# Performance work log

Measured on AMD Instinct MI355X. Metric: run time of the kernel, lower is better.

The kernel has to match this reference:

```python
import jax, jax.numpy as jnp
from jax import lax
import numpy as np


def _relu(x):
    return jnp.maximum(x, 0)


def setup_inputs() -> dict:
    key = jax.random.key(0)
    ks = jax.random.split(key, 20)
    B = 1024
    s = 0.05  # small init scale
    d = {
        "raw_input": jax.random.normal(ks[0], (B, 1, 28, 28), jnp.float32),
        "output_embed": jax.random.normal(ks[1], (B, 512), jnp.float32),
        "latent_embed": jax.random.normal(ks[2], (B, 512), jnp.float32),
        "conv1_w": jax.random.normal(ks[3], (16, 1, 3, 3), jnp.float32) * s,
        "conv1_b": jax.random.normal(ks[4], (16,), jnp.float32) * s,
        "conv2_w": jax.random.normal(ks[5], (32, 16, 3, 3), jnp.float32) * s,
        "conv2_b": jax.random.normal(ks[6], (32,), jnp.float32) * s,
        "proj_w1": jax.random.normal(ks[7], (1568, 1024), jnp.float32) * s,
        "proj_b1": jax.random.normal(ks[8], (1024,), jnp.float32) * s,
        "proj_w2": jax.random.normal(ks[9], (1024, 512), jnp.float32) * s,
        "proj_b2": jax.random.normal(ks[10], (512,), jnp.float32) * s,
        "bb_w1": jax.random.normal(ks[11], (512, 1024), jnp.float32) * s,
        "bb_b1": jax.random.normal(ks[12], (1024,), jnp.float32) * s,
        "bb_w2": jax.random.normal(ks[13], (1024, 512), jnp.float32) * s,
        "bb_b2": jax.random.normal(ks[14], (512,), jnp.float32) * s,
        "head_w": jax.random.normal(ks[15], (512, 10), jnp.float32) * s,
        "head_b": jax.random.normal(ks[16], (10,), jnp.float32) * s,
        "Nsup": 16,
        "n_latent": 6,
    }
    return d


def _maxpool2(x):
    # 2x2 max pool, stride 2, NCHW
    return lax.reduce_window(x, -jnp.inf, lax.max, (1, 1, 2, 2), (1, 1, 2, 2), "VALID")


def reference(raw_input, output_embed, latent_embed,
              conv1_w, conv1_b, conv2_w, conv2_b,
              proj_w1, proj_b1, proj_w2, proj_b2,
              bb_w1, bb_b1, bb_w2, bb_b2,
              head_w, head_b, Nsup, n_latent):
    dn = ("NCHW", "OIHW", "NCHW")
    B = raw_input.shape[0]

    def backbone(x):
        return _relu(_relu(x @ bb_w1 + bb_b1) @ bb_w2 + bb_b2)

    def latent_recursion(inp, out, lat, n):
        if n > 0:
            for _ in range(n):
                lat = backbone(inp + out + lat)
            out = backbone(lat + inp)
        else:
            out = backbone(inp + out + lat)
        return out, lat

    # CNN extractor + input embedding projection (B, 512)
    x = _relu(lax.conv_general_dilated(raw_input, conv1_w, (1, 1), "SAME",
                                       dimension_numbers=dn) + conv1_b[None, :, None, None])
    x = _maxpool2(x)  # (B,16,14,14)
    x = _relu(lax.conv_general_dilated(x, conv2_w, (1, 1), "SAME",
                                       dimension_numbers=dn) + conv2_b[None, :, None, None])
    x = _maxpool2(x)  # (B,32,7,7)
    h = x.reshape(B, -1)  # (B, 1568)
    inp = _relu(_relu(h @ proj_w1 + proj_b1) @ proj_w2 + proj_b2)  # (B,512)

    sg = lax.stop_gradient
    out, lat = output_embed, latent_embed
    T = 3
    logits = None
    for _ in range(Nsup):
        # deep_recursion: T-1 no-grad latent recursions, then one tracked
        for _ in range(T - 1):
            out, lat = latent_recursion(inp, out, lat, n_latent)
            out, lat = sg(out), sg(lat)
        out, lat = latent_recursion(inp, out, lat, n_latent)
        logits = out @ head_w + head_b
        out, lat = sg(out), sg(lat)
    return logits
```

## Files before the change

### kernel.cpp

```cpp
#include <hip/hip_runtime.h>
#include <hip/hip_bf16.h>


typedef unsigned short ushort_t;
typedef __attribute__((ext_vector_type(8))) short short8;
typedef __attribute__((ext_vector_type(4))) float f32x4;

__device__ inline unsigned f2bf_rne(float v) {
    unsigned u = __float_as_uint(v);
    return (u + 0x7fffu + ((u >> 16) & 1u)) >> 16;
}
__device__ inline void split2(float v, ushort_t& h, ushort_t& l) {
    unsigned uh = f2bf_rne(v);
    h = (ushort_t)uh;
    float fh = __uint_as_float(uh << 16);
    l = (ushort_t)f2bf_rne(v - fh);
}

__global__ __launch_bounds__(256) void conv1_pool(
    const float* __restrict__ in, const float* __restrict__ w,
    const float* __restrict__ bias, float* __restrict__ out)
{
    int idx = blockIdx.x * 256 + threadIdx.x;
    int xo = idx % 14; int t = idx / 14;
    int yo = t % 14;  t /= 14;
    int oc = t % 16;  int b = t / 16;
    const float* ip = in + (size_t)b * 784;
    const float* wp = w + oc * 9;
    float win[4][4];
#pragma unroll
    for (int yy = 0; yy < 4; ++yy)
#pragma unroll
        for (int xx = 0; xx < 4; ++xx) {
            int y = 2 * yo + yy - 1, x = 2 * xo + xx - 1;
            win[yy][xx] = (y >= 0 && y < 28 && x >= 0 && x < 28) ? ip[y * 28 + x] : 0.f;
        }
    float bs = bias[oc];
    float m = -1e30f;
#pragma unroll
    for (int py = 0; py < 2; ++py)
#pragma unroll
        for (int px = 0; px < 2; ++px) {
            float s = bs;
#pragma unroll
            for (int dy = 0; dy < 3; ++dy)
#pragma unroll
                for (int dx = 0; dx < 3; ++dx)
                    s = fmaf(win[py + dy][px + dx], wp[dy * 3 + dx], s);
            m = fmaxf(m, s);
        }
    out[idx] = fmaxf(m, 0.f);
}

__global__ __launch_bounds__(256) void conv2_pool(
    const float* __restrict__ in, const float* __restrict__ w,
    const float* __restrict__ bias, float* __restrict__ out)
{
    __shared__ float ws_[32 * 16 * 9];
    for (int i = threadIdx.x; i < 4608; i += 256) ws_[i] = w[i];
    __syncthreads();
    int idx = blockIdx.x * 256 + threadIdx.x;
    int xo = idx % 7; int t = idx / 7;
    int yo = t % 7;  t /= 7;
    int oc = t % 32; int b = t / 32;
    const float* ip = in + (size_t)b * 16 * 196;
    float bs = bias[oc];
    float s00 = bs, s01 = bs, s10 = bs, s11 = bs;
    for (int ic = 0; ic < 16; ++ic) {
        const float* ipp = ip + ic * 196;
        float win[4][4];
#pragma unroll
        for (int yy = 0; yy < 4; ++yy)
#pragma unroll
            for (int xx = 0; xx < 4; ++xx) {
                int y = 2 * yo + yy - 1, x = 2 * xo + xx - 1;
                win[yy][xx] = (y >= 0 && y < 14 && x >= 0 && x < 14) ? ipp[y * 14 + x] : 0.f;
            }
        const float* wp = ws_ + (oc * 16 + ic) * 9;
#pragma unroll
        for (int dy = 0; dy < 3; ++dy)
#pragma unroll
            for (int dx = 0; dx < 3; ++dx) {
                float wv = wp[dy * 3 + dx];
                s00 = fmaf(win[0 + dy][0 + dx], wv, s00);
                s01 = fmaf(win[0 + dy][1 + dx], wv, s01);
                s10 = fmaf(win[1 + dy][0 + dx], wv, s10);
                s11 = fmaf(win[1 + dy][1 + dx], wv, s11);
            }
    }
    float m = fmaxf(fmaxf(s00, s01), fmaxf(s10, s11));
    out[idx] = fmaxf(m, 0.f);
}

#define BMF 64
#define BNF 64
#define BKF 16

__global__ __launch_bounds__(256) void gemm_f32(
    const float* __restrict__ A0, const float* __restrict__ W,
    const float* __restrict__ bias, float* __restrict__ C,
    int M, int N, int K)
{
    __shared__ float As[BKF][BMF];
    __shared__ float Bs[BKF][BNF];
    const int tid = threadIdx.x;
    const int tx = tid % 16;
    const int ty = tid / 16;
    const int row0 = blockIdx.y * BMF;
    const int col0 = blockIdx.x * BNF;
    float acc[4][4] = {};
    const int ra = tid / 4;
    const int ca = 4 * (tid % 4);
    const int rb = tid / 16;
    const int cb = 4 * (tid % 16);
    for (int k0 = 0; k0 < K; k0 += BKF) {
        float4 v = *(const float4*)(A0 + (size_t)(row0 + ra) * K + k0 + ca);
        float4 bvec = *(const float4*)(W + (size_t)(k0 + rb) * N + col0 + cb);
        As[ca + 0][ra] = v.x;
        As[ca + 1][ra] = v.y;
        As[ca + 2][ra] = v.z;
        As[ca + 3][ra] = v.w;
        *(float4*)&Bs[rb][cb] = bvec;
        __syncthreads();
#pragma unroll
        for (int kk = 0; kk < BKF; ++kk) {
            float4 av = *(const float4*)&As[kk][ty * 4];
            float4 bv = *(const float4*)&Bs[kk][tx * 4];
            float a_[4] = {av.x, av.y, av.z, av.w};
            float b_[4] = {bv.x, bv.y, bv.z, bv.w};
#pragma unroll
            for (int i = 0; i < 4; ++i)
#pragma unroll
                for (int j = 0; j < 4; ++j)
                    acc[i][j] = fmaf(a_[i], b_[j], acc[i][j]);
        }
        __syncthreads();
    }
    float4 bv = *(const float4*)(bias + col0 + tx * 4);
    float bb[4] = {bv.x, bv.y, bv.z, bv.w};
#pragma unroll
    for (int i = 0; i < 4; ++i) {
        float4 o;
        o.x = fmaxf(acc[i][0] + bb[0], 0.f);
        o.y = fmaxf(acc[i][1] + bb[1], 0.f);
        o.z = fmaxf(acc[i][2] + bb[2], 0.f);
        o.w = fmaxf(acc[i][3] + bb[3], 0.f);
        *(float4*)(C + (size_t)(row0 + ty * 4 + i) * N + col0 + tx * 4) = o;
    }
}

__global__ __launch_bounds__(256) void prep_wt(
    const float* __restrict__ w, ushort_t* __restrict__ th,
    ushort_t* __restrict__ tl, int K, int N)
{
    int idx = blockIdx.x * 256 + threadIdx.x;
    int n = idx / K, k = idx % K;
    float v = w[(size_t)k * N + n];
    split2(v, th[idx], tl[idx]);
}

__global__ __launch_bounds__(256) void init_xs(
    const float* __restrict__ inpf, const float* __restrict__ oute,
    const float* __restrict__ late, float* __restrict__ io,
    ushort_t* __restrict__ xh, ushort_t* __restrict__ xl)
{
    int i = blockIdx.x * 256 + threadIdx.x;
    float t = inpf[i] + oute[i];
    io[i] = t;
    split2(t + late[i], xh[i], xl[i]);
}

__global__ void init_bar(unsigned* bar) {
    bar[threadIdx.x] = 0;
    bar[threadIdx.x + 256] = 0;
}

__device__ __forceinline__ void group_barrier(unsigned* bar, int g,
                                              unsigned& tgt)
{
    __syncthreads();
    if (threadIdx.x == 0) {
        __builtin_amdgcn_fence(__ATOMIC_RELEASE, "workgroup");
        __hip_atomic_fetch_add(bar + g * 32, 1u, __ATOMIC_RELAXED,
                               __HIP_MEMORY_SCOPE_AGENT);
        while (__hip_atomic_load(bar + g * 32, __ATOMIC_RELAXED,
                                 __HIP_MEMORY_SCOPE_AGENT) < tgt)
            __builtin_amdgcn_s_sleep(1);
        __builtin_amdgcn_fence(__ATOMIC_ACQUIRE, "workgroup");
        asm volatile("buffer_inv sc0" ::: "memory");
    }
    tgt += 32;
    __syncthreads();
}

__device__ __forceinline__ short8 afrag(const ushort_t* __restrict__ p,
                                        int row, int K, int kpos)
{
    return *(const short8*)(p + (size_t)row * K + kpos);
}

__global__ __launch_bounds__(512, 2) void trm_persist(
    ushort_t* __restrict__ xs_hi, ushort_t* __restrict__ xs_lo,
    ushort_t* __restrict__ h1_hi, ushort_t* __restrict__ h1_lo,
    const ushort_t* __restrict__ W1h, const ushort_t* __restrict__ W1l,
    const ushort_t* __restrict__ W2h, const ushort_t* __restrict__ W2l,
    const float* __restrict__ bb1, const float* __restrict__ bb2,
    float* __restrict__ io, const float* __restrict__ inpf,
    float* __restrict__ latf, float* __restrict__ outf,
    const float* __restrict__ hw, const float* __restrict__ hb,
    float* __restrict__ logits, unsigned* bar)
{
    __shared__ __align__(16) unsigned char w1lds[65536];
    __shared__ __align__(16) unsigned char w2lds[65536];
    __shared__ int sh_gs;

    const int tid = threadIdx.x;
    const int w = tid >> 6, lane = tid & 63;
    const int q = lane >> 4, li = lane & 15;

    if (tid == 0) {
        unsigned xcc;
        asm volatile("s_getreg_b32 %0, hwreg(HW_REG_XCC_ID)" : "=s"(xcc));
        xcc &= 7u;
        unsigned s = __hip_atomic_fetch_add(bar + 384 + xcc * 8, 1u,
                                            __ATOMIC_RELAXED,
                                            __HIP_MEMORY_SCOPE_AGENT);
        sh_gs = (int)((xcc << 8) | (s & 31u));
    }
    __syncthreads();
    const int g = sh_gs >> 8;
    const int slot = sh_gs & 255;
    const int c1 = slot * 32;
    const int c2 = slot * 16;
    const int rowA = g * 128 + w * 16;

    for (int i = tid; i < 4096; i += 512) {
        int comp = i >> 11;
        int rem = i & 2047;
        int n = rem >> 6, c = rem & 63;
        const ushort_t* src = (comp ? W1l : W1h) + (size_t)(c1 + n) * 512 + c * 8;
        int dst = ((((comp << 4) + (c >> 2)) * 2 + (n >> 4)) * 64 +
                   ((c & 3) * 16 + (n & 15))) * 16;
        *(uint4*)(w1lds + dst) = *(const uint4*)src;
    }
    for (int i = tid; i < 4096; i += 512) {
        int comp = i >> 11;
        int rem = i & 2047;
        int n = rem >> 7, c = rem & 127;
        const ushort_t* src = (comp ? W2l : W2h) + (size_t)(c2 + n) * 1024 + c * 8;
        int dst = (((comp << 5) + (c >> 2)) * 64 + ((c & 3) * 16 + n)) * 16;
        *(uint4*)(w2lds + dst) = *(const uint4*)src;
    }
    __syncthreads();

    float bias1[2];
    bias1[0] = bb1[c1 + li];
    bias1[1] = bb1[c1 + 16 + li];
    float bias2 = bb2[c2 + li];
    unsigned tgt = 32;

    for (int step = 0; step < 336; ++step) {
        {
            f32x4 acc0 = {}, acc1 = {};
            short8 aF[4][2];
#pragma unroll
            for (int p = 0; p < 4; ++p) {
                int kp = p * 32 + q * 8;
                aF[p][0] = afrag(xs_hi, rowA + li, 512, kp);
                aF[p][1] = afrag(xs_lo, rowA + li, 512, kp);
            }
#pragma unroll
            for (int s = 0; s < 16; ++s) {
                short8 ah = aF[s & 3][0], al = aF[s & 3][1];
                if (s + 4 < 16) {
                    int kp = (s + 4) * 32 + q * 8;
                    aF[(s + 4) & 3][0] = afrag(xs_hi, rowA + li, 512, kp);
                    aF[(s + 4) & 3][1] = afrag(xs_lo, rowA + li, 512, kp);
                }
                const int base = (s * 2 * 64 + lane) * 16;
                short8 bh0 = *(const short8*)(w1lds + base);
                short8 bh1 = *(const short8*)(w1lds + base + 1024);
                short8 bl0 = *(const short8*)(w1lds + 32768 + base);
                short8 bl1 = *(const short8*)(w1lds + 32768 + base + 1024);
                acc0 = __builtin_amdgcn_mfma_f32_16x16x32_bf16(ah, bh0, acc0, 0, 0, 0);
                acc0 = __builtin_amdgcn_mfma_f32_16x16x32_bf16(ah, bl0, acc0, 0, 0, 0);
                acc0 = __builtin_amdgcn_mfma_f32_16x16x32_bf16(al, bh0, acc0, 0, 0, 0);
                acc0 = __builtin_amdgcn_mfma_f32_16x16x32_bf16(al, bl0, acc0, 0, 0, 0);
                acc1 = __builtin_amdgcn_mfma_f32_16x16x32_bf16(ah, bh1, acc1, 0, 0, 0);
                acc1 = __builtin_amdgcn_mfma_f32_16x16x32_bf16(ah, bl1, acc1, 0, 0, 0);
                acc1 = __builtin_amdgcn_mfma_f32_16x16x32_bf16(al, bh1, acc1, 0, 0, 0);
                acc1 = __builtin_amdgcn_mfma_f32_16x16x32_bf16(al, bl1, acc1, 0, 0, 0);
            }
#pragma unroll
            for (int tj = 0; tj < 2; ++tj) {
                int colg = c1 + tj * 16 + li;
                float bv = bias1[tj];
#pragma unroll
                for (int rr = 0; rr < 4; ++rr) {
                    int rowg = rowA + q * 4 + rr;
                    size_t idx = (size_t)rowg * 1024 + colg;
                    float v = fmaxf((tj ? acc1[rr] : acc0[rr]) + bv, 0.f);
                    split2(v, h1_hi[idx], h1_lo[idx]);
                }
            }
        }
        group_barrier(bar, g, tgt);

        {
            int im = step % 7;
            int mode = (im < 5) ? 1 : ((im == 5) ? 2 : 3);
            f32x4 acc = {};
            short8 aF[4][2];
#pragma unroll
            for (int p = 0; p < 4; ++p) {
                int kp = p * 32 + q * 8;
                aF[p][0] = afrag(h1_hi, rowA + li, 1024, kp);
                aF[p][1] = afrag(h1_lo, rowA + li, 1024, kp);
            }
#pragma unroll
            for (int s = 0; s < 32; ++s) {
                short8 ah = aF[s & 3][0], al = aF[s & 3][1];
                if (s + 4 < 32) {
                    int kp = (s + 4) * 32 + q * 8;
                    aF[(s + 4) & 3][0] = afrag(h1_hi, rowA + li, 1024, kp);
                    aF[(s + 4) & 3][1] = afrag(h1_lo, rowA + li, 1024, kp);
                }
                const int base = (s * 64 + lane) * 16;
                short8 bh = *(const short8*)(w2lds + base);
                short8 bl = *(const short8*)(w2lds + 32768 + base);
                acc = __builtin_amdgcn_mfma_f32_16x16x32_bf16(ah, bh, acc, 0, 0, 0);
                acc = __builtin_amdgcn_mfma_f32_16x16x32_bf16(ah, bl, acc, 0, 0, 0);
                acc = __builtin_amdgcn_mfma_f32_16x16x32_bf16(al, bh, acc, 0, 0, 0);
                acc = __builtin_amdgcn_mfma_f32_16x16x32_bf16(al, bl, acc, 0, 0, 0);
            }
            int colg = c2 + li;
#pragma unroll
            for (int rr = 0; rr < 4; ++rr) {
                int rowg = rowA + q * 4 + rr;
                size_t idx = (size_t)rowg * 512 + colg;
                float v = fmaxf(acc[rr] + bias2, 0.f);
                if (mode == 1) {
                    split2(io[idx] + v, xs_hi[idx], xs_lo[idx]);
                } else if (mode == 2) {
                    split2(inpf[idx] + v, xs_hi[idx], xs_lo[idx]);
                    latf[idx] = v;
                } else {
                    outf[idx] = v;
                    float t2 = inpf[idx] + v;
                    io[idx] = t2;
                    split2(t2 + latf[idx], xs_hi[idx], xs_lo[idx]);
                }
            }
        }
        group_barrier(bar, g, tgt);
    }

    {
        int idx = slot * 512 + tid;
        if (idx < 1280) {
            int rloc = idx / 10, j = idx % 10;
            int row = g * 128 + rloc;
            const float* r = outf + (size_t)row * 512;
            float s = hb[j];
            for (int k = 0; k < 512; ++k) s = fmaf(r[k], hw[k * 10 + j], s);
            logits[row * 10 + j] = s;
        }
    }
}

extern "C" void kernel_launch(void* const* d_in, const int* in_sizes, int n_in,
                              void* d_out, int out_size, void* d_ws, size_t ws_size,
                              hipStream_t stream)
{
    const float* raw   = (const float*)d_in[0];
    const float* out_e = (const float*)d_in[1];
    const float* lat_e = (const float*)d_in[2];
    const float* c1w = (const float*)d_in[3];
    const float* c1b = (const float*)d_in[4];
    const float* c2w = (const float*)d_in[5];
    const float* c2b = (const float*)d_in[6];
    const float* pw1 = (const float*)d_in[7];
    const float* pb1 = (const float*)d_in[8];
    const float* pw2 = (const float*)d_in[9];
    const float* pb2 = (const float*)d_in[10];
    const float* bw1 = (const float*)d_in[11];
    const float* bb1 = (const float*)d_in[12];
    const float* bw2 = (const float*)d_in[13];
    const float* bb2 = (const float*)d_in[14];
    const float* hw  = (const float*)d_in[15];
    const float* hb  = (const float*)d_in[16];

    char* base = (char*)d_ws;
    float*    pool1  = (float*)   (base + 0);
    ushort_t* h1_hi  = (ushort_t*)(base + 0);
    ushort_t* h1_lo  = (ushort_t*)(base + 2097152);
    ushort_t* xs_hi  = (ushort_t*)(base + 4194304);
    ushort_t* xs_lo  = (ushort_t*)(base + 5242880);
    float*    io     = (float*)   (base + 6291456);
    float*    latf   = (float*)   (base + 8388608);
    float*    h1f    = (float*)   (base + 0);
    float*    h      = (float*)   (base + 12845056);
    float*    inpf   = (float*)   (base + 19267584);
    float*    outf   = (float*)   (base + 21364736);
    ushort_t* bW1t_h = (ushort_t*)(base + 23461888);
    ushort_t* bW1t_l = (ushort_t*)(base + 24510464);
    ushort_t* bW2t_h = (ushort_t*)(base + 25559040);
    ushort_t* bW2t_l = (ushort_t*)(base + 26607616);
    unsigned* bar    = (unsigned*)(base + 27656192);

    prep_wt<<<2048, 256, 0, stream>>>(bw1, bW1t_h, bW1t_l, 512, 1024);
    prep_wt<<<2048, 256, 0, stream>>>(bw2, bW2t_h, bW2t_l, 1024, 512);
    init_bar<<<1, 256, 0, stream>>>(bar);

    conv1_pool<<<3211264 / 256, 256, 0, stream>>>(raw, c1w, c1b, pool1);
    conv2_pool<<<1605632 / 256, 256, 0, stream>>>(pool1, c2w, c2b, h);
    gemm_f32<<<dim3(16, 16), 256, 0, stream>>>(h, pw1, pb1, h1f, 1024, 1024, 1568);
    gemm_f32<<<dim3(8, 16), 256, 0, stream>>>(h1f, pw2, pb2, inpf, 1024, 512, 1024);
    init_xs<<<2048, 256, 0, stream>>>(inpf, out_e, lat_e, io, xs_hi, xs_lo);

    trm_persist<<<256, 512, 0, stream>>>(
        xs_hi, xs_lo, h1_hi, h1_lo, bW1t_h, bW1t_l, bW2t_h, bW2t_l,
        bb1, bb2, io, inpf, latf, outf, hw, hb, (float*)d_out, bar);
}
```

Before: 8.440 ms.

## Pack hi/lo bf16 activations interleaved and drop lo*lo MFMA term

Activation hi/lo bf16 splits are now stored interleaved in one 32-bit word per element, so each fragment comes from a single contiguous global load and is unpacked with byte permutes. The lo*lo product term, which contributes negligibly to the result, is also dropped from both backbone GEMMs, cutting MFMA count per k-step from 4 to 3. Each unpack adds some VALU work, and accuracy drops slightly.

```diff
diff --git a/kernel.cpp b/kernel.cpp
--- a/kernel.cpp
+++ b/kernel.cpp
@@ -15,6 +15,31 @@
     h = (ushort_t)uh;
     float fh = __uint_as_float(uh << 16);
     l = (ushort_t)f2bf_rne(v - fh);
+}
+__device__ inline unsigned split2pk(float v) {
+    unsigned uh = f2bf_rne(v);
+    float fh = __uint_as_float(uh << 16);
+    unsigned ul = f2bf_rne(v - fh);
+    return (ul << 16) | uh;
+}
+
+union S8U { short8 s; unsigned u[4]; };
+__device__ __forceinline__ void unpk(uint4 u0, uint4 u1, short8& h, short8& l) {
+    S8U a, b;
+    a.u[0] = __builtin_amdgcn_perm(u0.y, u0.x, 0x05040100u);
+    b.u[0] = __builtin_amdgcn_perm(u0.y, u0.x, 0x07060302u);
+    a.u[1] = __builtin_amdgcn_perm(u0.w, u0.z, 0x05040100u);
+    b.u[1] = __builtin_amdgcn_perm(u0.w, u0.z, 0x07060302u);
+    a.u[2] = __builtin_amdgcn_perm(u1.y, u1.x, 0x05040100u);
+    b.u[2] = __builtin_amdgcn_perm(u1.y, u1.x, 0x07060302u);
+    a.u[3] = __builtin_amdgcn_perm(u1.w, u1.z, 0x05040100u);
+    b.u[3] = __builtin_amdgcn_perm(u1.w, u1.z, 0x07060302u);
+    h = a.s; l = b.s;
+}
+__device__ __forceinline__ void ldpk(const unsigned* __restrict__ p, int row,
+                                     int K, int kpos, uint4& u0, uint4& u1) {
+    const uint4* q = (const uint4*)(p + (size_t)row * K + kpos);
+    u0 = q[0]; u1 = q[1];
 }
 
 __global__ __launch_bounds__(256) void conv1_pool(
@@ -162,12 +187,12 @@
 __global__ __launch_bounds__(256) void init_xs(
     const float* __restrict__ inpf, const float* __restrict__ oute,
     const float* __restrict__ late, float* __restrict__ io,
-    ushort_t* __restrict__ xh, ushort_t* __restrict__ xl)
+    unsigned* __restrict__ xs_pk)
 {
     int i = blockIdx.x * 256 + threadIdx.x;
     float t = inpf[i] + oute[i];
     io[i] = t;
-    split2(t + late[i], xh[i], xl[i]);
+    xs_pk[i] = split2pk(t + late[i]);
 }
 
 __global__ void init_bar(unsigned* bar) {
@@ -193,15 +218,8 @@
     __syncthreads();
 }
 
-__device__ __forceinline__ short8 afrag(const ushort_t* __restrict__ p,
-                                        int row, int K, int kpos)
-{
-    return *(const short8*)(p + (size_t)row * K + kpos);
-}
-
 __global__ __launch_bounds__(512, 2) void trm_persist(
-    ushort_t* __restrict__ xs_hi, ushort_t* __restrict__ xs_lo,
-    ushort_t* __restrict__ h1_hi, ushort_t* __restrict__ h1_lo,
+    unsigned* __restrict__ xs_pk, unsigned* __restrict__ h1_pk,
     const ushort_t* __restrict__ W1h, const ushort_t* __restrict__ W1l,
     const ushort_t* __restrict__ W2h, const ushort_t* __restrict__ W2l,
     const float* __restrict__ bb1, const float* __restrict__ bb2,
@@ -262,21 +280,17 @@
     for (int step = 0; step < 336; ++step) {
         {
             f32x4 acc0 = {}, acc1 = {};
-            short8 aF[4][2];
-#pragma unroll
-            for (int p = 0; p < 4; ++p) {
-                int kp = p * 32 + q * 8;
-                aF[p][0] = afrag(xs_hi, rowA + li, 512, kp);
-                aF[p][1] = afrag(xs_lo, rowA + li, 512, kp);
-            }
+            uint4 aR[4][2];
+#pragma unroll
+            for (int p = 0; p < 4; ++p)
+                ldpk(xs_pk, rowA + li, 512, p * 32 + q * 8, aR[p][0], aR[p][1]);
 #pragma unroll
             for (int s = 0; s < 16; ++s) {
-                short8 ah = aF[s & 3][0], al = aF[s & 3][1];
-                if (s + 4 < 16) {
-                    int kp = (s + 4) * 32 + q * 8;
-                    aF[(s + 4) & 3][0] = afrag(xs_hi, rowA + li, 512, kp);
-                    aF[(s + 4) & 3][1] = afrag(xs_lo, rowA + li, 512, kp);
-                }
+                short8 ah, al;
+                unpk(aR[s & 3][0], aR[s & 3][1], ah, al);
+                if (s + 4 < 16)
+                    ldpk(xs_pk, rowA + li, 512, (s + 4) * 32 + q * 8,
+                         aR[(s + 4) & 3][0], aR[(s + 4) & 3][1]);
                 const int base = (s * 2 * 64 + lane) * 16;
                 short8 bh0 = *(const short8*)(w1lds + base);
                 short8 bh1 = *(const short8*)(w1lds + base + 1024);
@@ -285,11 +299,9 @@
                 acc0 = __builtin_amdgcn_mfma_f32_16x16x32_bf16(ah, bh0, acc0, 0, 0, 0);
                 acc0 = __builtin_amdgcn_mfma_f32_16x16x32_bf16(ah, bl0, acc0, 0, 0, 0);
                 acc0 = __builtin_amdgcn_mfma_f32_16x16x32_bf16(al, bh0, acc0, 0, 0, 0);
-                acc0 = __builtin_amdgcn_mfma_f32_16x16x32_bf16(al, bl0, acc0, 0, 0, 0);
                 acc1 = __builtin_amdgcn_mfma_f32_16x16x32_bf16(ah, bh1, acc1, 0, 0, 0);
                 acc1 = __builtin_amdgcn_mfma_f32_16x16x32_bf16(ah, bl1, acc1, 0, 0, 0);
                 acc1 = __builtin_amdgcn_mfma_f32_16x16x32_bf16(al, bh1, acc1, 0, 0, 0);
-                acc1 = __builtin_amdgcn_mfma_f32_16x16x32_bf16(al, bl1, acc1, 0, 0, 0);
             }
 #pragma unroll
             for (int tj = 0; tj < 2; ++tj) {
@@ -300,7 +312,7 @@
                     int rowg = rowA + q * 4 + rr;
                     size_t idx = (size_t)rowg * 1024 + colg;
                     float v = fmaxf((tj ? acc1[rr] : acc0[rr]) + bv, 0.f);
-                    split2(v, h1_hi[idx], h1_lo[idx]);
+                    h1_pk[idx] = split2pk(v);
                 }
             }
         }
@@ -310,28 +322,23 @@
             int im = step % 7;
             int mode = (im < 5) ? 1 : ((im == 5) ? 2 : 3);
             f32x4 acc = {};
-            short8 aF[4][2];
-#pragma unroll
-            for (int p = 0; p < 4; ++p) {
-                int kp = p * 32 + q * 8;
-                aF[p][0] = afrag(h1_hi, rowA + li, 1024, kp);
-                aF[p][1] = afrag(h1_lo, rowA + li, 1024, kp);
-            }
+            uint4 aR[4][2];
+#pragma unroll
+            for (int p = 0; p < 4; ++p)
+                ldpk(h1_pk, rowA + li, 1024, p * 32 + q * 8, aR[p][0], aR[p][1]);
 #pragma unroll
             for (int s = 0; s < 32; ++s) {
-                short8 ah = aF[s & 3][0], al = aF[s & 3][1];
-                if (s + 4 < 32) {
-                    int kp = (s + 4) * 32 + q * 8;
-                    aF[(s + 4) & 3][0] = afrag(h1_hi, rowA + li, 1024, kp);
-                    aF[(s + 4) & 3][1] = afrag(h1_lo, rowA + li, 1024, kp);
-                }
+                short8 ah, al;
+                unpk(aR[s & 3][0], aR[s & 3][1], ah, al);
+                if (s + 4 < 32)
+                    ldpk(h1_pk, rowA + li, 1024, (s + 4) * 32 + q * 8,
+                         aR[(s + 4) & 3][0], aR[(s + 4) & 3][1]);
                 const int base = (s * 64 + lane) * 16;
                 short8 bh = *(const short8*)(w2lds + base);
                 short8 bl = *(const short8*)(w2lds + 32768 + base);
                 acc = __builtin_amdgcn_mfma_f32_16x16x32_bf16(ah, bh, acc, 0, 0, 0);
                 acc = __builtin_amdgcn_mfma_f32_16x16x32_bf16(ah, bl, acc, 0, 0, 0);
                 acc = __builtin_amdgcn_mfma_f32_16x16x32_bf16(al, bh, acc, 0, 0, 0);
-                acc = __builtin_amdgcn_mfma_f32_16x16x32_bf16(al, bl, acc, 0, 0, 0);
             }
             int colg = c2 + li;
 #pragma unroll
@@ -340,15 +347,15 @@
                 size_t idx = (size_t)rowg * 512 + colg;
                 float v = fmaxf(acc[rr] + bias2, 0.f);
                 if (mode == 1) {
-                    split2(io[idx] + v, xs_hi[idx], xs_lo[idx]);
+                    xs_pk[idx] = split2pk(io[idx] + v);
                 } else if (mode == 2) {
-                    split2(inpf[idx] + v, xs_hi[idx], xs_lo[idx]);
+                    xs_pk[idx] = split2pk(inpf[idx] + v);
                     latf[idx] = v;
                 } else {
                     outf[idx] = v;
                     float t2 = inpf[idx] + v;
                     io[idx] = t2;
-                    split2(t2 + latf[idx], xs_hi[idx], xs_lo[idx]);
+                    xs_pk[idx] = split2pk(t2 + latf[idx]);
                 }
             }
         }
@@ -392,10 +399,8 @@
 
     char* base = (char*)d_ws;
     float*    pool1  = (float*)   (base + 0);
-    ushort_t* h1_hi  = (ushort_t*)(base + 0);
-    ushort_t* h1_lo  = (ushort_t*)(base + 2097152);
-    ushort_t* xs_hi  = (ushort_t*)(base + 4194304);
-    ushort_t* xs_lo  = (ushort_t*)(base + 5242880);
+    unsigned* h1_pk  = (unsigned*)(base + 0);
+    unsigned* xs_pk  = (unsigned*)(base + 4194304);
     float*    io     = (float*)   (base + 6291456);
     float*    latf   = (float*)   (base + 8388608);
     float*    h1f    = (float*)   (base + 0);
@@ -416,9 +421,9 @@
     conv2_pool<<<1605632 / 256, 256, 0, stream>>>(pool1, c2w, c2b, h);
     gemm_f32<<<dim3(16, 16), 256, 0, stream>>>(h, pw1, pb1, h1f, 1024, 1024, 1568);
     gemm_f32<<<dim3(8, 16), 256, 0, stream>>>(h1f, pw2, pb2, inpf, 1024, 512, 1024);
-    init_xs<<<2048, 256, 0, stream>>>(inpf, out_e, lat_e, io, xs_hi, xs_lo);
+    init_xs<<<2048, 256, 0, stream>>>(inpf, out_e, lat_e, io, xs_pk);
 
     trm_persist<<<256, 512, 0, stream>>>(
-        xs_hi, xs_lo, h1_hi, h1_lo, bW1t_h, bW1t_l, bW2t_h, bW2t_l,
+        xs_pk, h1_pk, bW1t_h, bW1t_l, bW2t_h, bW2t_l,
         bb1, bb2, io, inpf, latf, outf, hw, hb, (float*)d_out, bar);
 }
```

After: 8.455 ms. No clear change (+0.2%).
